# Kernel optimization log

Measured on AMD Instinct MI355X. Metric: run time of the kernel, lower is better.

## Reference

```python
import jax, jax.numpy as jnp
import numpy as np

N_ATOMS, N_EDGES = 8192, 131072
NODE_DIM, HIDDEN_DIM, NUM_BASIS, N_BLOCKS, N_SPECIES = 128, 64, 20, 2, 100
CUTOFF = 5.0


def setup_inputs() -> dict:
    key = jax.random.key(0)
    ks = iter(jax.random.split(key, 40))
    F, H, NB, B, Z = NODE_DIM, HIDDEN_DIM, NUM_BASIS, N_BLOCKS, N_SPECIES

    def w(k, shape, fan_in):
        return jax.random.normal(k, shape, jnp.float32) / np.float32(np.sqrt(fan_in))

    inp = {
        "at_no": jax.random.randint(next(ks), (N_ATOMS,), 1, 86),
        "coord": jax.random.uniform(next(ks), (N_ATOMS, 3), jnp.float32) * 5.0,
        "edge_index": jax.random.randint(next(ks), (2, N_EDGES), 0, N_ATOMS),
        "charge": 0,
        "spin": 0,
        # learned parameters
        "emb": w(next(ks), (Z, F), 1.0),
        "atom_sp": w(next(ks), (Z,), 1.0),
        "msg_w1": w(next(ks), (B, F, F), F), "msg_b1": jnp.zeros((B, F), jnp.float32),
        "msg_w2": w(next(ks), (B, F, 3 * F), F), "msg_b2": jnp.zeros((B, 3 * F), jnp.float32),
        "msg_wr": w(next(ks), (B, NB, 3 * F), NB), "msg_br": jnp.zeros((B, 3 * F), jnp.float32),
        "upd_u": w(next(ks), (B, F, F), F), "upd_v": w(next(ks), (B, F, F), F),
        "upd_w1": w(next(ks), (B, 2 * F, F), 2 * F), "upd_b1": jnp.zeros((B, F), jnp.float32),
        "upd_w2": w(next(ks), (B, F, 3 * F), F), "upd_b2": jnp.zeros((B, 3 * F), jnp.float32),
        "out_w1": w(next(ks), (F, H), F), "out_b1": jnp.zeros((H,), jnp.float32),
        "out_w2": w(next(ks), (H, 1), H), "out_b2": jnp.zeros((1,), jnp.float32),
    }
    return inp


def _painn_energy(coord, at_no, edge_index, emb, atom_sp,
                  msg_w1, msg_b1, msg_w2, msg_b2, msg_wr, msg_br,
                  upd_u, upd_v, upd_w1, upd_b1, upd_w2, upd_b2,
                  out_w1, out_b1, out_w2, out_b2):
    n_atoms = coord.shape[0]
    n_blocks = msg_w1.shape[0]
    nb = msg_wr.shape[1]
    rc = jnp.asarray(CUTOFF, coord.dtype)
    src, dst = edge_index[0], edge_index[1]

    rij = coord[dst] - coord[src]                       # [E,3]
    d = jnp.sqrt(jnp.sum(rij * rij, -1) + 1e-12)        # [E]
    unit = rij / d[:, None]                             # [E,3] (l=1 real sph. harmonics up to const)
    n = jnp.arange(1, nb + 1, dtype=coord.dtype)
    rbf = jnp.sqrt(2.0 / rc) * jnp.sin(n[None, :] * jnp.pi * d[:, None] / rc) / d[:, None]  # Bessel RBF [E,NB]
    fcut = jnp.where(d < rc, 0.5 * (jnp.cos(jnp.pi * d / rc) + 1.0), 0.0)                   # cosine cutoff [E]

    x = emb[at_no]                                      # [N,F]
    v = jnp.zeros((n_atoms, 3, x.shape[1]), x.dtype)    # [N,3,F]

    for b in range(n_blocks):
        # ---- PaiNN message block ----
        phi = jax.nn.silu(x @ msg_w1[b] + msg_b1[b]) @ msg_w2[b] + msg_b2[b]   # [N,3F]
        filt = (rbf @ msg_wr[b] + msg_br[b]) * fcut[:, None]                   # [E,3F]
        m = phi[src] * filt                                                    # [E,3F]
        ds, dv1, dv2 = jnp.split(m, 3, axis=-1)
        dvec = dv1[:, None, :] * v[src] + dv2[:, None, :] * unit[:, :, None]   # [E,3,F]
        x = x + jax.ops.segment_sum(ds, dst, num_segments=n_atoms)
        v = v + jax.ops.segment_sum(dvec, dst, num_segments=n_atoms)
        # ---- PaiNN update block ----
        uv = jnp.einsum('nif,fg->nig', v, upd_u[b])
        vv = jnp.einsum('nif,fg->nig', v, upd_v[b])
        vnorm = jnp.sqrt(jnp.sum(vv * vv, axis=1) + 1e-12)                     # [N,F]
        a = jax.nn.silu(jnp.concatenate([x, vnorm], -1) @ upd_w1[b] + upd_b1[b]) @ upd_w2[b] + upd_b2[b]
        a_vv, a_sv, a_ss = jnp.split(a, 3, axis=-1)
        v = v + a_vv[:, None, :] * uv
        x = x + a_sv * jnp.sum(uv * vv, axis=1) + a_ss

    atom_e = jax.nn.silu(x @ out_w1 + out_b1) @ out_w2 + out_b2                # [N,1]
    return jnp.sum(atom_e) + jnp.sum(atom_sp[at_no])


def reference(at_no, coord, edge_index, charge, spin, emb, atom_sp,
              msg_w1, msg_b1, msg_w2, msg_b2, msg_wr, msg_br,
              upd_u, upd_v, upd_w1, upd_b1, upd_w2, upd_b2,
              out_w1, out_b1, out_w2, out_b2):
    def energy_fn(c):
        return _painn_energy(c, at_no, edge_index, emb, atom_sp,
                             msg_w1, msg_b1, msg_w2, msg_b2, msg_wr, msg_br,
                             upd_u, upd_v, upd_w1, upd_b1, upd_w2, upd_b2,
                             out_w1, out_b1, out_w2, out_b2)
    energy, nuc_grad = jax.value_and_grad(energy_fn)(coord)
    return energy, nuc_grad
```

## Files before the change

### kernel.cpp

```cpp
#include <hip/hip_runtime.h>
#include <math.h>


#define NA 8192
#define NE 131072
#define FD 128
#define FD3 384
#define NBASE 20
#define HD 64
#define RCUT 5.0f
#define PIF 3.14159265358979f

typedef short bf16x8 __attribute__((ext_vector_type(8)));
typedef float f32x4 __attribute__((ext_vector_type(4)));
typedef _Float16 f16x2 __attribute__((ext_vector_type(2)));

static __device__ __forceinline__ float silu_f(float x) {
    return x / (1.f + expf(-x));
}
static __device__ __forceinline__ float dsilu_f(float x) {
    float s = 1.f / (1.f + expf(-x));
    return s * (1.f + x * (1.f - s));
}
static __device__ __forceinline__ short f2bf(float x) {
    union { float f; unsigned int i; } c; c.f = x;
    unsigned int r = c.i + 0x7fffu + ((c.i >> 16) & 1u);
    return (short)(r >> 16);
}
static __device__ __forceinline__ float bf2f(short u) {
    union { unsigned int i; float f; } c; c.i = ((unsigned int)(unsigned short)u) << 16; return c.f;
}
static __device__ __forceinline__ float dot2f(f16x2 a, f16x2 b, float c) {
#if __has_builtin(__builtin_amdgcn_fdot2)
    return __builtin_amdgcn_fdot2(a, b, c, false);
#else
    return c + (float)a.x * (float)b.x + (float)a.y * (float)b.y;
#endif
}
static __device__ __forceinline__ unsigned int packf16(float a, float b) {
    union { _Float16 h[2]; unsigned int u; } c;
    c.h[0] = (_Float16)a; c.h[1] = (_Float16)b;
    return c.u;
}

__global__ __launch_bounds__(256) void mfma_gemm_kernel(
    const float* __restrict__ A, const float* __restrict__ W,
    const float* __restrict__ bias, const float* __restrict__ dsil,
    const float* __restrict__ addbuf, float* __restrict__ C,
    int M, int N, int K, int asilu, int acc, int wtrans)
{
    __shared__ short AsH[128][40];
    __shared__ short AsL[128][40];
    __shared__ short WsH[64][40];
    __shared__ short WsL[64][40];
    int tid = threadIdx.x;
    int row0 = blockIdx.y * 128, col0 = blockIdx.x * 64;
    int wv = tid >> 6, lane = tid & 63;
    int quad = lane >> 4, l16 = lane & 15;

    f32x4 accv[2][4];
    #pragma unroll
    for (int i = 0; i < 2; ++i)
        #pragma unroll
        for (int j = 0; j < 4; ++j) { f32x4 z = {0.f, 0.f, 0.f, 0.f}; accv[i][j] = z; }

    int am = tid >> 1;
    int ak = (tid & 1) * 16;
    const float* abase = A + (size_t)(row0 + am) * K + ak;
    int wn = tid & 63, wk0 = tid >> 6;
    int wk2 = tid & 31, wn2 = tid >> 5;

    for (int k0 = 0; k0 < K; k0 += 32) {
        {
            const float* ap = abase + k0;
            #pragma unroll
            for (int i = 0; i < 4; ++i) {
                float4 v = *(const float4*)(ap + 4 * i);
                if (asilu) {
                    v.x = silu_f(v.x); v.y = silu_f(v.y);
                    v.z = silu_f(v.z); v.w = silu_f(v.w);
                }
                float vv[4] = {v.x, v.y, v.z, v.w};
                #pragma unroll
                for (int q = 0; q < 4; ++q) {
                    short h = f2bf(vv[q]);
                    AsH[am][ak + 4 * i + q] = h;
                    AsL[am][ak + 4 * i + q] = f2bf(vv[q] - bf2f(h));
                }
            }
        }
        if (!wtrans) {
            #pragma unroll
            for (int p = 0; p < 8; ++p) {
                int k = wk0 + p * 4;
                float v = W[(size_t)(k0 + k) * N + col0 + wn];
                short h = f2bf(v);
                WsH[wn][k] = h;
                WsL[wn][k] = f2bf(v - bf2f(h));
            }
        } else {
            #pragma unroll
            for (int p = 0; p < 8; ++p) {
                int n2 = wn2 + p * 8;
                float v = W[(size_t)(col0 + n2) * K + k0 + wk2];
                short h = f2bf(v);
                WsH[n2][wk2] = h;
                WsL[n2][wk2] = f2bf(v - bf2f(h));
            }
        }
        __syncthreads();
        bf16x8 afH[2], afL[2], bfH[4], bfL[4];
        #pragma unroll
        for (int rt = 0; rt < 2; ++rt) {
            afH[rt] = *(const bf16x8*)&AsH[wv * 32 + rt * 16 + l16][quad * 8];
            afL[rt] = *(const bf16x8*)&AsL[wv * 32 + rt * 16 + l16][quad * 8];
        }
        #pragma unroll
        for (int ct = 0; ct < 4; ++ct) {
            bfH[ct] = *(const bf16x8*)&WsH[ct * 16 + l16][quad * 8];
            bfL[ct] = *(const bf16x8*)&WsL[ct * 16 + l16][quad * 8];
        }
        #pragma unroll
        for (int rt = 0; rt < 2; ++rt)
            #pragma unroll
            for (int ct = 0; ct < 4; ++ct) {
                accv[rt][ct] = __builtin_amdgcn_mfma_f32_16x16x32_bf16(
                    afL[rt], bfH[ct], accv[rt][ct], 0, 0, 0);
                accv[rt][ct] = __builtin_amdgcn_mfma_f32_16x16x32_bf16(
                    afH[rt], bfL[ct], accv[rt][ct], 0, 0, 0);
                accv[rt][ct] = __builtin_amdgcn_mfma_f32_16x16x32_bf16(
                    afH[rt], bfH[ct], accv[rt][ct], 0, 0, 0);
            }
        __syncthreads();
    }
    #pragma unroll
    for (int rt = 0; rt < 2; ++rt) {
        #pragma unroll
        for (int ct = 0; ct < 4; ++ct) {
            int colv = col0 + ct * 16 + l16;
            float bv = bias ? bias[colv] : 0.f;
            #pragma unroll
            for (int r = 0; r < 4; ++r) {
                int rowv = row0 + wv * 32 + rt * 16 + quad * 4 + r;
                float v = accv[rt][ct][r] + bv;
                size_t idx = (size_t)rowv * N + colv;
                if (dsil) { float pz = dsil[idx]; float s = 1.f / (1.f + expf(-pz)); v *= s * (1.f + pz * (1.f - s)); }
                if (addbuf) v += addbuf[idx];
                if (acc) C[idx] += v; else C[idx] = v;
            }
        }
    }
}

__global__ void embed_kernel(const int* at_no, const float* emb, float* x) {
    int i = blockIdx.x * blockDim.x + threadIdx.x;
    int n = i >> 7, f = i & 127;
    x[i] = emb[(size_t)at_no[n] * FD + f];
}

__global__ void combo_prep_kernel(const float* u, const float* v, float* UVcomb, float* Tcomb) {
    int i = blockIdx.x * blockDim.x + threadIdx.x;
    {
        int k = i >> 8, j = i & 255;
        UVcomb[i] = (j < 128) ? u[k * 128 + j] : v[k * 128 + (j - 128)];
    }
    {
        int k = i >> 7, j = i & 127;
        Tcomb[i] = (k < 128) ? u[j * 128 + k] : v[j * 128 + (k - 128)];
    }
}

__global__ void wpack_kernel(const float* __restrict__ Wr, unsigned int* __restrict__ out) {
    int i = blockIdx.x * blockDim.x + threadIdx.x;
    if (i >= 3840) return;
    int k2 = i / 384, r = i - k2 * 384;
    out[i] = packf16(Wr[(2 * k2) * FD3 + r], Wr[(2 * k2 + 1) * FD3 + r]);
}

__global__ void geom_fwd_kernel(const float* coord, const int* ei,
    float* d_e, float* unit_e, float* rbf_e, float* drbf_e, float* fcut_e, float* dfc_e,
    unsigned int* rbfh_e, unsigned int* drbfh_e,
    int* cnt_dst, int* cnt_src)
{
    int e = blockIdx.x * blockDim.x + threadIdx.x;
    if (e >= NE) return;
    int s = ei[e], t = ei[NE + e];
    atomicAdd(&cnt_src[s], 1);
    atomicAdd(&cnt_dst[t], 1);
    float rx = coord[t * 3 + 0] - coord[s * 3 + 0];
    float ry = coord[t * 3 + 1] - coord[s * 3 + 1];
    float rz = coord[t * 3 + 2] - coord[s * 3 + 2];
    float r2 = rx * rx + ry * ry + rz * rz;
    float dd = sqrtf(r2 + 1e-12f);
    float inv = 1.f / dd;
    d_e[e] = dd;
    unit_e[e * 3 + 0] = rx * inv; unit_e[e * 3 + 1] = ry * inv; unit_e[e * 3 + 2] = rz * inv;
    const float c0 = 0.6324555320336759f;
    float rb[NBASE], db[NBASE];
    for (int k = 0; k < NBASE; ++k) {
        float nk = (k + 1) * (PIF / RCUT);
        float sn, cs; sincosf(nk * dd, &sn, &cs);
        rb[k] = c0 * sn * inv;
        db[k] = c0 * (nk * cs * inv - sn * inv * inv);
        rbf_e[(size_t)e * NBASE + k] = rb[k];
        drbf_e[(size_t)e * NBASE + k] = db[k];
    }
    #pragma unroll
    for (int k2 = 0; k2 < 10; ++k2) {
        rbfh_e[(size_t)e * 10 + k2] = packf16(rb[2 * k2], rb[2 * k2 + 1]);
        drbfh_e[(size_t)e * 10 + k2] = packf16(db[2 * k2], db[2 * k2 + 1]);
    }
    if (dd < RCUT) {
        float sn, cs; sincosf(PIF * dd / RCUT, &sn, &cs);
        fcut_e[e] = 0.5f * (cs + 1.f);
        dfc_e[e] = -0.5f * (PIF / RCUT) * sn;
    } else { fcut_e[e] = 0.f; dfc_e[e] = 0.f; }
}

__global__ __launch_bounds__(1024) void scan_kernel(
    const int* cnt_dst, const int* cnt_src,
    int* off_dst, int* off_src, int* cur_dst, int* cur_src)
{
    __shared__ int part[1024];
    const int* cnt = (blockIdx.x == 0) ? cnt_dst : cnt_src;
    int* off = (blockIdx.x == 0) ? off_dst : off_src;
    int* cur = (blockIdx.x == 0) ? cur_dst : cur_src;
    int t = threadIdx.x;
    int base = t * 8;
    int loc[8]; int s = 0;
    #pragma unroll
    for (int i = 0; i < 8; ++i) { loc[i] = s; s += cnt[base + i]; }
    part[t] = s;
    __syncthreads();
    for (int d = 1; d < 1024; d <<= 1) {
        int v = part[t];
        int w = (t >= d) ? part[t - d] : 0;
        __syncthreads();
        part[t] = v + w;
        __syncthreads();
    }
    int pre = (t == 0) ? 0 : part[t - 1];
    #pragma unroll
    for (int i = 0; i < 8; ++i) { int o = pre + loc[i]; off[base + i] = o; cur[base + i] = o; }
    if (t == 1023) off[NA] = part[1023];
}

__global__ void scatter_kernel(const int* ei, int* cur_dst, int* cur_src,
                               int* perm_dst, int* perm_src, int* srcp, int* dstp) {
    int e = blockIdx.x * blockDim.x + threadIdx.x;
    if (e >= NE) return;
    int s = ei[e], t = ei[NE + e];
    int pd = atomicAdd(&cur_dst[t], 1); perm_dst[pd] = e; srcp[pd] = s;
    int ps = atomicAdd(&cur_src[s], 1); perm_src[ps] = e; dstp[ps] = t;
}

__global__ __launch_bounds__(256) void msg_fwd_kernel(
    const int* __restrict__ row_off_dst, const int* __restrict__ perm_dst, const int* __restrict__ srcp,
    const unsigned int* __restrict__ rbfh_e, const float* __restrict__ fcut_e, const float* __restrict__ unit_e,
    const float* __restrict__ phi, const unsigned int* __restrict__ Wrp, const float* __restrict__ br,
    const float* __restrict__ x_in, const float* __restrict__ v_in,
    float* __restrict__ x_mid, float* __restrict__ v_mid)
{
    int tid = threadIdx.x;
    int n = blockIdx.x * 2 + (tid >> 7);
    int f = tid & 127;
    f16x2 w0[10], w1[10], w2[10];
    #pragma unroll
    for (int k2 = 0; k2 < 10; ++k2) {
        unsigned int a = Wrp[k2 * 384 + f];
        unsigned int b = Wrp[k2 * 384 + 128 + f];
        unsigned int c = Wrp[k2 * 384 + 256 + f];
        w0[k2] = *(const f16x2*)&a;
        w1[k2] = *(const f16x2*)&b;
        w2[k2] = *(const f16x2*)&c;
    }
    float b0 = br[f], b1 = br[FD + f], b2 = br[2 * FD + f];
    float xa = 0.f, va0 = 0.f, va1 = 0.f, va2 = 0.f;
    int e0 = row_off_dst[n], e1 = row_off_dst[n + 1];
    for (int ii = e0; ii < e1; ++ii) {
        int e = perm_dst[ii];
        int s = srcp[ii];
        float fc = fcut_e[e];
        float raw0 = b0, raw1 = b1, raw2 = b2;
        #pragma unroll
        for (int k2 = 0; k2 < 10; ++k2) {
            unsigned int ra = rbfh_e[(size_t)e * 10 + k2];
            f16x2 r = *(const f16x2*)&ra;
            raw0 = dot2f(r, w0[k2], raw0);
            raw1 = dot2f(r, w1[k2], raw1);
            raw2 = dot2f(r, w2[k2], raw2);
        }
        float f0 = raw0 * fc, f1 = raw1 * fc, f2 = raw2 * fc;
        const float* ph = phi + (size_t)s * FD3;
        float m0 = ph[f] * f0, m1 = ph[FD + f] * f1, m2 = ph[2 * FD + f] * f2;
        xa += m0;
        float u0 = unit_e[e * 3], u1 = unit_e[e * 3 + 1], u2 = unit_e[e * 3 + 2];
        float vs0 = 0.f, vs1 = 0.f, vs2 = 0.f;
        if (v_in) {
            const float* vp = v_in + (size_t)s * 3 * FD;
            vs0 = vp[f]; vs1 = vp[FD + f]; vs2 = vp[2 * FD + f];
        }
        va0 += m1 * vs0 + m2 * u0;
        va1 += m1 * vs1 + m2 * u1;
        va2 += m1 * vs2 + m2 * u2;
    }
    size_t xb = (size_t)n * FD + f;
    x_mid[xb] = x_in[xb] + xa;
    size_t vb = (size_t)n * 3 * FD + f;
    float p0 = 0.f, p1 = 0.f, p2 = 0.f;
    if (v_in) { p0 = v_in[vb]; p1 = v_in[vb + FD]; p2 = v_in[vb + 2 * FD]; }
    v_mid[vb] = p0 + va0; v_mid[vb + FD] = p1 + va1; v_mid[vb + 2 * FD] = p2 + va2;
}

__global__ void vnorm_cat_kernel(const float* xmid, const float* uvvv, float* vnorm, float* cat) {
    int i = blockIdx.x * blockDim.x + threadIdx.x;
    int n = i >> 7, g = i & 127;
    size_t ub = (size_t)n * 3 * 256 + 128 + g;
    float a = uvvv[ub], b = uvvv[ub + 256], c = uvvv[ub + 512];
    float vn = sqrtf(a * a + b * b + c * c + 1e-12f);
    vnorm[i] = vn;
    cat[(size_t)n * 2 * FD + g] = xmid[i];
    cat[(size_t)n * 2 * FD + FD + g] = vn;
}

__global__ void combine_kernel(const float* xmid, const float* vmid,
    const float* uvvv, const float* a_,
    float* x_out, float* v_out )
{
    int i = blockIdx.x * blockDim.x + threadIdx.x;
    int n = i >> 7, g = i & 127;
    size_t vb = (size_t)n * 3 * FD + g;
    size_t ub = (size_t)n * 3 * 256 + g;
    float uv0 = uvvv[ub], uv1 = uvvv[ub + 256], uv2 = uvvv[ub + 512];
    float vv0 = uvvv[ub + 128], vv1 = uvvv[ub + 384], vv2 = uvvv[ub + 640];
    float S = uv0 * vv0 + uv1 * vv1 + uv2 * vv2;
    const float* ar = a_ + (size_t)n * FD3;
    x_out[i] = xmid[i] + ar[FD + g] * S + ar[2 * FD + g];
    if (v_out) {
        float avv = ar[g];
        v_out[vb] = vmid[vb] + avv * uv0;
        v_out[vb + FD] = vmid[vb + FD] + avv * uv1;
        v_out[vb + 2 * FD] = vmid[vb + 2 * FD] + avv * uv2;
    }
}

__global__ __launch_bounds__(256) void energy_kernel(
    const float* tout, const float* ow2, const float* ob2,
    const float* atom_sp, const int* at_no, float* out)
{
    int n = blockIdx.x * 256 + threadIdx.x;
    float e = ob2[0] + atom_sp[at_no[n]];
    for (int h = 0; h < HD; ++h) {
        float t = tout[(size_t)n * HD + h];
        e = fmaf(silu_f(t), ow2[h], e);
    }
    #pragma unroll
    for (int off = 32; off > 0; off >>= 1) e += __shfl_down(e, off);
    __shared__ float s[4];
    int lane = threadIdx.x & 63, wv = threadIdx.x >> 6;
    if (lane == 0) s[wv] = e;
    __syncthreads();
    if (threadIdx.x == 0) atomicAdd(out, s[0] + s[1] + s[2] + s[3]);
}

__global__ __launch_bounds__(128) void head_bwd_kernel(
    const float* tout, const float* ow1, const float* ow2, float* gx)
{
    __shared__ float sh[HD];
    int n = blockIdx.x, f = threadIdx.x;
    if (f < HD) {
        float p = tout[(size_t)n * HD + f];
        sh[f] = dsilu_f(p) * ow2[f];
    }
    __syncthreads();
    float g = 0.f;
    #pragma unroll
    for (int h = 0; h < HD; ++h) g = fmaf(sh[h], ow1[f * HD + h], g);
    gx[(size_t)n * FD + f] = g;
}

__global__ void ubwd1_kernel(const float* gx, const float* gv,
    const float* uvvv, float* g_a)
{
    int i = blockIdx.x * blockDim.x + threadIdx.x;
    int n = i >> 7, g = i & 127;
    size_t vb = (size_t)n * 3 * FD + g;
    size_t ub = (size_t)n * 3 * 256 + g;
    float uv0 = uvvv[ub], uv1 = uvvv[ub + 256], uv2 = uvvv[ub + 512];
    float vv0 = uvvv[ub + 128], vv1 = uvvv[ub + 384], vv2 = uvvv[ub + 640];
    float gv0 = gv[vb], gv1 = gv[vb + FD], gv2 = gv[vb + 2 * FD];
    float gxv = gx[i];
    float S = uv0 * vv0 + uv1 * vv1 + uv2 * vv2;
    size_t ab = (size_t)n * FD3;
    g_a[ab + g]           = gv0 * uv0 + gv1 * uv1 + gv2 * uv2;
    g_a[ab + FD + g]      = gxv * S;
    g_a[ab + 2 * FD + g]  = gxv;
}

__global__ void ubwd2_kernel(const float* gx_in, const float* gv_in,
    const float* a_, const float* vnorm, const float* g_cat,
    float* uvvv, float* gx_mid, float* gv_tmp)
{
    int i = blockIdx.x * blockDim.x + threadIdx.x;
    int n = i >> 7, g = i & 127;
    size_t vb = (size_t)n * 3 * FD + g, ab = (size_t)n * FD3;
    size_t ub = (size_t)n * 3 * 256 + g;
    float gxv = gx_in[i];
    float gS = gxv * a_[ab + FD + g];
    float avv = a_[ab + g];
    float gvn = g_cat[(size_t)n * 2 * FD + FD + g];
    float c = gvn / vnorm[i];
    float uv0 = uvvv[ub], uv1 = uvvv[ub + 256], uv2 = uvvv[ub + 512];
    float vv0 = uvvv[ub + 128], vv1 = uvvv[ub + 384], vv2 = uvvv[ub + 640];
    float gv0 = gv_in[vb], gv1 = gv_in[vb + FD], gv2 = gv_in[vb + 2 * FD];
    uvvv[ub]       = gv0 * avv + gS * vv0;
    uvvv[ub + 256] = gv1 * avv + gS * vv1;
    uvvv[ub + 512] = gv2 * avv + gS * vv2;
    uvvv[ub + 128] = gS * uv0 + c * vv0;
    uvvv[ub + 384] = gS * uv1 + c * vv1;
    uvvv[ub + 640] = gS * uv2 + c * vv2;
    gv_tmp[vb] = gv0; gv_tmp[vb + FD] = gv1; gv_tmp[vb + 2 * FD] = gv2;
    gx_mid[i] = gxv + g_cat[(size_t)n * 2 * FD + g];
}

__global__ __launch_bounds__(256) void msg_bwd_merged_kernel(
    const int* __restrict__ row_off_src, const int* __restrict__ perm_src, const int* __restrict__ dstp,
    const unsigned int* __restrict__ rbfh_e, const unsigned int* __restrict__ drbfh_e,
    const float* __restrict__ fcut_e, const float* __restrict__ dfc_e,
    const float* __restrict__ unit_e,
    const float* phi, const unsigned int* __restrict__ Wrp, const float* __restrict__ br,
    const float* __restrict__ v_in,
    const float* __restrict__ gx_mid, const float* __restrict__ gv_mid,
    float* gphi_out,
    float* __restrict__ gv_out,
    float* __restrict__ gd_e, float* __restrict__ gu_e)
{
    __shared__ float red[12][4][64];
    int tid = threadIdx.x;
    int wv = tid >> 6, lane = tid & 63;
    int n = blockIdx.x;
    f16x2 w[2][3][10];
    float brv[2][3], ph[2][3], vs[2][3];
    #pragma unroll
    for (int h = 0; h < 2; ++h) {
        int f = lane + h * 64;
        #pragma unroll
        for (int s = 0; s < 3; ++s) {
            #pragma unroll
            for (int k2 = 0; k2 < 10; ++k2) {
                unsigned int u = Wrp[k2 * 384 + s * 128 + f];
                w[h][s][k2] = *(const f16x2*)&u;
            }
            brv[h][s] = br[s * FD + f];
            ph[h][s] = phi[(size_t)n * FD3 + s * FD + f];
            vs[h][s] = v_in ? v_in[(size_t)n * 3 * FD + s * FD + f] : 0.f;
        }
    }
    float gp[2][3] = {{0.f, 0.f, 0.f}, {0.f, 0.f, 0.f}};
    float ga[2][3] = {{0.f, 0.f, 0.f}, {0.f, 0.f, 0.f}};
    int e0 = row_off_src[n], e1 = row_off_src[n + 1];
    for (int ii = e0 + wv; ii < e1; ii += 4) {
        int e = perm_src[ii], dd = dstp[ii];
        float fc = fcut_e[e], dfc = dfc_e[e];
        float u0 = unit_e[e * 3], u1 = unit_e[e * 3 + 1], u2 = unit_e[e * 3 + 2];
        f16x2 rb2[10], db2[10];
        #pragma unroll
        for (int k2 = 0; k2 < 10; ++k2) {
            unsigned int ra = rbfh_e[(size_t)e * 10 + k2];
            unsigned int db = drbfh_e[(size_t)e * 10 + k2];
            rb2[k2] = *(const f16x2*)&ra;
            db2[k2] = *(const f16x2*)&db;
        }
        float r0 = 0.f, r1 = 0.f, r2 = 0.f, r3 = 0.f;
        #pragma unroll
        for (int h = 0; h < 2; ++h) {
            int f = lane + h * 64;
            float raw0 = brv[h][0], raw1 = brv[h][1], raw2 = brv[h][2];
            float A0 = 0.f, A1 = 0.f, A2 = 0.f;
            #pragma unroll
            for (int k2 = 0; k2 < 10; ++k2) {
                raw0 = dot2f(rb2[k2], w[h][0][k2], raw0);
                raw1 = dot2f(rb2[k2], w[h][1][k2], raw1);
                raw2 = dot2f(rb2[k2], w[h][2][k2], raw2);
                A0 = dot2f(db2[k2], w[h][0][k2], A0);
                A1 = dot2f(db2[k2], w[h][1][k2], A1);
                A2 = dot2f(db2[k2], w[h][2][k2], A2);
            }
            float f0 = raw0 * fc, f1 = raw1 * fc, f2 = raw2 * fc;
            float gds = gx_mid[(size_t)dd * FD + f];
            const float* gvp = gv_mid + (size_t)dd * 3 * FD;
            float gd0 = gvp[f], gd1 = gvp[FD + f], gd2 = gvp[2 * FD + f];
            float gdv1 = gd0 * vs[h][0] + gd1 * vs[h][1] + gd2 * vs[h][2];
            float gdv2 = gd0 * u0 + gd1 * u1 + gd2 * u2;
            float dv1 = ph[h][1] * f1;
            ga[h][0] += gd0 * dv1; ga[h][1] += gd1 * dv1; ga[h][2] += gd2 * dv1;
            gp[h][0] += gds * f0; gp[h][1] += gdv1 * f1; gp[h][2] += gdv2 * f2;
            float dv2 = ph[h][2] * f2;
            r1 += gd0 * dv2; r2 += gd1 * dv2; r3 += gd2 * dv2;
            float gf0 = gds * ph[h][0], gf1 = gdv1 * ph[h][1], gf2 = gdv2 * ph[h][2];
            r0 += fc * (gf0 * A0 + gf1 * A1 + gf2 * A2)
                + dfc * (gf0 * raw0 + gf1 * raw1 + gf2 * raw2);
        }
        #pragma unroll
        for (int off = 32; off > 0; off >>= 1) {
            r0 += __shfl_down(r0, off);
            r1 += __shfl_down(r1, off);
            r2 += __shfl_down(r2, off);
            r3 += __shfl_down(r3, off);
        }
        if (lane == 0) {
            gd_e[e] += r0;
            gu_e[e * 3]     += r1;
            gu_e[e * 3 + 1] += r2;
            gu_e[e * 3 + 2] += r3;
        }
    }
    #pragma unroll
    for (int h = 0; h < 2; ++h)
        #pragma unroll
        for (int s = 0; s < 3; ++s) {
            red[h * 3 + s][wv][lane] = gp[h][s];
            red[6 + h * 3 + s][wv][lane] = ga[h][s];
        }
    __syncthreads();
    int j0 = tid >> 6;
    #pragma unroll
    for (int rep = 0; rep < 3; ++rep) {
        int j = j0 + rep * 4;
        float v = red[j][0][lane] + red[j][1][lane] + red[j][2][lane] + red[j][3][lane];
        int jj = (j < 6) ? j : j - 6;
        int h = jj / 3, s = jj - 3 * h;
        int f = h * 64 + lane;
        if (j < 6) {
            gphi_out[(size_t)n * FD3 + s * FD + f] = v;
        } else {
            size_t vb = (size_t)n * 3 * FD + s * FD + f;
            gv_out[vb] = gv_mid[vb] + v;
        }
    }
}

__global__ void edge_vec_kernel(const float* coord, const int* ei,
    const float* d_e, const float* gd_e, const float* gu_e, float* gvec)
{
    int e = blockIdx.x * blockDim.x + threadIdx.x;
    if (e >= NE) return;
    int s = ei[e], t = ei[NE + e];
    float rx = coord[t * 3 + 0] - coord[s * 3 + 0];
    float ry = coord[t * 3 + 1] - coord[s * 3 + 1];
    float rz = coord[t * 3 + 2] - coord[s * 3 + 2];
    float dd = d_e[e];
    float inv = 1.f / dd;
    float gu0 = gu_e[e * 3], gu1 = gu_e[e * 3 + 1], gu2 = gu_e[e * 3 + 2];
    float gd = gd_e[e];
    float dot = gu0 * rx + gu1 * ry + gu2 * rz;
    float coef = gd * inv - dot * inv * inv * inv;
    gvec[e * 3 + 0] = gu0 * inv + coef * rx;
    gvec[e * 3 + 1] = gu1 * inv + coef * ry;
    gvec[e * 3 + 2] = gu2 * inv + coef * rz;
}

__global__ __launch_bounds__(256) void coord_gather_kernel(
    const int* __restrict__ off_dst, const int* __restrict__ perm_dst,
    const int* __restrict__ off_src, const int* __restrict__ perm_src,
    const float* __restrict__ gvec, float* __restrict__ gcoord)
{
    int n = blockIdx.x * 4 + (threadIdx.x >> 6);
    int lane = threadIdx.x & 63;
    float a0 = 0.f, a1 = 0.f, a2 = 0.f;
    int d0 = off_dst[n], d1 = off_dst[n + 1];
    for (int ii = d0 + lane; ii < d1; ii += 64) {
        int e = perm_dst[ii];
        a0 += gvec[e * 3]; a1 += gvec[e * 3 + 1]; a2 += gvec[e * 3 + 2];
    }
    int s0 = off_src[n], s1 = off_src[n + 1];
    for (int ii = s0 + lane; ii < s1; ii += 64) {
        int e = perm_src[ii];
        a0 -= gvec[e * 3]; a1 -= gvec[e * 3 + 1]; a2 -= gvec[e * 3 + 2];
    }
    #pragma unroll
    for (int off = 32; off > 0; off >>= 1) {
        a0 += __shfl_down(a0, off);
        a1 += __shfl_down(a1, off);
        a2 += __shfl_down(a2, off);
    }
    if (lane == 0) {
        gcoord[n * 3 + 0] = a0; gcoord[n * 3 + 1] = a1; gcoord[n * 3 + 2] = a2;
    }
}

extern "C" void kernel_launch(void* const* d_in, const int* in_sizes, int n_in,
                              void* d_out, int out_size, void* d_ws, size_t ws_size,
                              hipStream_t stream)
{
    (void)in_sizes; (void)n_in; (void)out_size; (void)ws_size;
    const int*   at_no   = (const int*)  d_in[0];
    const float* coord   = (const float*)d_in[1];
    const int*   eidx    = (const int*)  d_in[2];
    const float* emb     = (const float*)d_in[5];
    const float* atom_sp = (const float*)d_in[6];
    const float* msg_w1  = (const float*)d_in[7];
    const float* msg_b1  = (const float*)d_in[8];
    const float* msg_w2  = (const float*)d_in[9];
    const float* msg_b2  = (const float*)d_in[10];
    const float* msg_wr  = (const float*)d_in[11];
    const float* msg_br  = (const float*)d_in[12];
    const float* upd_u   = (const float*)d_in[13];
    const float* upd_v   = (const float*)d_in[14];
    const float* upd_w1  = (const float*)d_in[15];
    const float* upd_b1  = (const float*)d_in[16];
    const float* upd_w2  = (const float*)d_in[17];
    const float* upd_b2  = (const float*)d_in[18];
    const float* out_w1  = (const float*)d_in[19];
    const float* out_b1  = (const float*)d_in[20];
    const float* out_w2  = (const float*)d_in[21];
    const float* out_b2  = (const float*)d_in[22];
    float* out = (float*)d_out;
    float* gcoord = out + 1;

    char* wp = (char*)d_ws;
    auto alloc = [&](size_t nelem) -> float* {
        float* r = (float*)wp; wp += ((nelem * 4 + 255) & ~(size_t)255); return r;
    };
    auto alloci = [&](size_t nelem) -> int* {
        int* r = (int*)wp; wp += ((nelem * 4 + 255) & ~(size_t)255); return r;
    };
    auto allocu = [&](size_t nelem) -> unsigned int* {
        unsigned int* r = (unsigned int*)wp; wp += ((nelem * 4 + 255) & ~(size_t)255); return r;
    };
    const size_t NF = (size_t)NA * FD;

    float* d_e    = alloc(NE);
    float* unit_e = alloc(3 * (size_t)NE);
    float* rbf_e  = alloc((size_t)NBASE * NE);
    float* drbf_e = alloc((size_t)NBASE * NE);
    float* fcut_e = alloc(NE);
    float* dfc_e  = alloc(NE);
    float* gd_e   = alloc(NE);
    float* gu_e   = alloc(3 * (size_t)NE);
    unsigned int* rbfh_e  = allocu((size_t)10 * NE);
    unsigned int* drbfh_e = allocu((size_t)10 * NE);
    int* cnt_dst = alloci(NA); int* cnt_src = alloci(NA);
    int* off_dst = alloci(NA + 1); int* off_src = alloci(NA + 1);
    int* cur_dst = alloci(NA); int* cur_src = alloci(NA);
    int* perm_dst = alloci(NE); int* perm_src = alloci(NE);
    int* srcp = alloci(NE); int* dstp = alloci(NE);
    float* xin_all = alloc(3 * NF);
    float* xin0 = xin_all; float* xin1 = xin_all + NF; float* xfin = xin_all + 2 * NF;
    float* vout0 = alloc(3 * NF);
    float* xmid = alloc(NF);
    float* vmid = alloc(3 * NF);
    float* catb = alloc(2 * NF);
    float* toutb = alloc((size_t)NA * HD);
    float *s1b[2], *phib[2], *uvvv[2], *vnb[2], *t1b[2], *ab[2];
    for (int b = 0; b < 2; ++b) {
        s1b[b] = alloc(NF); phib[b] = alloc(3 * NF); uvvv[b] = alloc(6 * NF);
        vnb[b] = alloc(NF); t1b[b] = alloc(NF); ab[b] = alloc(3 * NF);
    }
    float* gxA = alloc(NF); float* gxB = alloc(NF);
    float* gvA = alloc(3 * NF);
    float* g_a   = xin_all;
    float* g_cat = catb;
    float* g_t1  = xmid;
    float* g_s1  = s1b[0];
    float* gvec_e = gu_e;
    float *UVcomb[2], *Tcomb[2];
    for (int b = 0; b < 2; ++b) { UVcomb[b] = alloc(FD * 256); Tcomb[b] = alloc(256 * FD); }
    unsigned int* Wrp[2];
    for (int b = 0; b < 2; ++b) Wrp[b] = allocu(3840);

    hipMemsetAsync(d_out, 0, (size_t)(1 + NA * 3) * 4, stream);
    hipMemsetAsync(cnt_dst, 0, (size_t)NA * 4, stream);
    hipMemsetAsync(cnt_src, 0, (size_t)NA * 4, stream);
    hipMemsetAsync(gd_e, 0, (size_t)NE * 4, stream);
    hipMemsetAsync(gu_e, 0, 3ull * NE * 4, stream);
    hipMemsetAsync(gvA, 0, 3 * NF * 4, stream);

    geom_fwd_kernel<<<NE / 256, 256, 0, stream>>>(coord, eidx, d_e, unit_e, rbf_e, drbf_e,
                                                  fcut_e, dfc_e, rbfh_e, drbfh_e, cnt_dst, cnt_src);
    scan_kernel<<<2, 1024, 0, stream>>>(cnt_dst, cnt_src, off_dst, off_src, cur_dst, cur_src);
    scatter_kernel<<<NE / 256, 256, 0, stream>>>(eidx, cur_dst, cur_src, perm_dst, perm_src, srcp, dstp);
    embed_kernel<<<NF / 256, 256, 0, stream>>>(at_no, emb, xin0);
    for (int b = 0; b < 2; ++b) {
        combo_prep_kernel<<<128, 256, 0, stream>>>(upd_u + (size_t)b * FD * FD,
                                                   upd_v + (size_t)b * FD * FD, UVcomb[b], Tcomb[b]);
        wpack_kernel<<<15, 256, 0, stream>>>(msg_wr + (size_t)b * NBASE * FD3, Wrp[b]);
    }

    auto gemm = [&](const float* A, const float* W, const float* bias, const float* dsil,
                    const float* addb, float* C, int M, int Nn, int K, int asilu, int acc, int wtrans) {
        dim3 g(Nn / 64, M / 128);
        mfma_gemm_kernel<<<g, 256, 0, stream>>>(A, W, bias, dsil, addb, C, M, Nn, K, asilu, acc, wtrans);
    };

    for (int b = 0; b < 2; ++b) {
        const float* xinb = b ? xin1 : xin0;
        const float* vin  = b ? vout0 : nullptr;
        gemm(xinb, msg_w1 + (size_t)b * FD * FD, msg_b1 + b * FD, nullptr, nullptr, s1b[b], NA, FD, FD, 0, 0, 0);
        gemm(s1b[b], msg_w2 + (size_t)b * FD * FD3, msg_b2 + b * FD3, nullptr, nullptr, phib[b], NA, FD3, FD, 1, 0, 0);
        msg_fwd_kernel<<<NA / 2, 256, 0, stream>>>(off_dst, perm_dst, srcp, rbfh_e, fcut_e, unit_e,
                                              phib[b], Wrp[b], msg_br + (size_t)b * FD3,
                                              xinb, vin, xmid, vmid);
        gemm(vmid, UVcomb[b], nullptr, nullptr, nullptr, uvvv[b], 3 * NA, 256, FD, 0, 0, 0);
        vnorm_cat_kernel<<<NF / 256, 256, 0, stream>>>(xmid, uvvv[b], vnb[b], catb);
        gemm(catb, upd_w1 + (size_t)b * 2 * FD * FD, upd_b1 + b * FD, nullptr, nullptr, t1b[b], NA, FD, 2 * FD, 0, 0, 0);
        gemm(t1b[b], upd_w2 + (size_t)b * FD * FD3, upd_b2 + b * FD3, nullptr, nullptr, ab[b], NA, FD3, FD, 1, 0, 0);
        combine_kernel<<<NF / 256, 256, 0, stream>>>(xmid, vmid, uvvv[b], ab[b],
                                                     b ? xfin : xin1, b ? nullptr : vout0);
    }
    gemm(xfin, out_w1, out_b1, nullptr, nullptr, toutb, NA, HD, FD, 0, 0, 0);
    energy_kernel<<<NA / 256, 256, 0, stream>>>(toutb, out_w2, out_b2, atom_sp, at_no, out);

    head_bwd_kernel<<<NA, FD, 0, stream>>>(toutb, out_w1, out_w2, gxA);
    for (int b = 1; b >= 0; --b) {
        ubwd1_kernel<<<NF / 256, 256, 0, stream>>>(gxA, gvA, uvvv[b], g_a);
        gemm(g_a, upd_w2 + (size_t)b * FD * FD3, nullptr, t1b[b], nullptr, g_t1, NA, FD, FD3, 0, 0, 1);
        gemm(g_t1, upd_w1 + (size_t)b * 2 * FD * FD, nullptr, nullptr, nullptr, g_cat, NA, 2 * FD, FD, 0, 0, 1);
        ubwd2_kernel<<<NF / 256, 256, 0, stream>>>(gxA, gvA, ab[b], vnb[b], g_cat,
                                                   uvvv[b], gxB, vmid);
        gemm(uvvv[b], Tcomb[b], nullptr, nullptr, nullptr, vmid, 3 * NA, FD, 256, 0, 1, 0);
        msg_bwd_merged_kernel<<<NA, 256, 0, stream>>>(off_src, perm_src, dstp,
                                              rbfh_e, drbfh_e, fcut_e, dfc_e, unit_e,
                                              phib[b], Wrp[b], msg_br + (size_t)b * FD3,
                                              b ? vout0 : nullptr, gxB, vmid,
                                              phib[b], gvA, gd_e, gu_e);
        if (b == 1) {
            gemm(phib[b], msg_w2 + (size_t)b * FD * FD3, nullptr, s1b[b], nullptr, g_s1, NA, FD, FD3, 0, 0, 1);
            gemm(g_s1, msg_w1 + (size_t)b * FD * FD, nullptr, nullptr, gxB, gxA, NA, FD, FD, 0, 0, 1);
        }
    }
    edge_vec_kernel<<<NE / 256, 256, 0, stream>>>(coord, eidx, d_e, gd_e, gu_e, gvec_e);
    coord_gather_kernel<<<NA / 4, 256, 0, stream>>>(off_dst, perm_dst, off_src, perm_src, gvec_e, gcoord);
}
```

Baseline: 1.165 ms.

## Add 64-row GEMM tile for small-N GEMMs and pack edge geometry into float4

Adds a 64x64-tile split-bf16 MFMA GEMM, used for the M=8192, N<=128 GEMMs, so these small GEMMs launch more blocks and fill more of the GPU's compute units. Packs each edge's unit vector and cutoff into one float4, so the message kernels fetch them with a single vector load instead of four scattered loads. Stops writing the fp32 rbf/drbf arrays, which no kernel reads, cutting geometry-kernel store traffic. The smaller tile reuses each loaded weight tile across fewer rows.

```diff
diff --git a/kernel.cpp b/kernel.cpp
--- a/kernel.cpp
+++ b/kernel.cpp
@@ -152,6 +152,103 @@
     }
 }
 
+__global__ __launch_bounds__(256) void mfma_gemm64_kernel(
+    const float* __restrict__ A, const float* __restrict__ W,
+    const float* __restrict__ bias, const float* __restrict__ dsil,
+    const float* __restrict__ addbuf, float* __restrict__ C,
+    int M, int N, int K, int asilu, int acc, int wtrans)
+{
+    __shared__ short AsH[64][40];
+    __shared__ short AsL[64][40];
+    __shared__ short WsH[64][40];
+    __shared__ short WsL[64][40];
+    int tid = threadIdx.x;
+    int row0 = blockIdx.y * 64, col0 = blockIdx.x * 64;
+    int wv = tid >> 6, lane = tid & 63;
+    int quad = lane >> 4, l16 = lane & 15;
+
+    f32x4 accv[4];
+    #pragma unroll
+    for (int j = 0; j < 4; ++j) { f32x4 z = {0.f, 0.f, 0.f, 0.f}; accv[j] = z; }
+
+    int am = tid >> 2;
+    int ak = (tid & 3) * 8;
+    const float* abase = A + (size_t)(row0 + am) * K + ak;
+    int wn = tid & 63, wk0 = tid >> 6;
+    int wk2 = tid & 31, wn2 = tid >> 5;
+
+    for (int k0 = 0; k0 < K; k0 += 32) {
+        {
+            const float* ap = abase + k0;
+            #pragma unroll
+            for (int i = 0; i < 2; ++i) {
+                float4 v = *(const float4*)(ap + 4 * i);
+                if (asilu) {
+                    v.x = silu_f(v.x); v.y = silu_f(v.y);
+                    v.z = silu_f(v.z); v.w = silu_f(v.w);
+                }
+                float vv[4] = {v.x, v.y, v.z, v.w};
+                #pragma unroll
+                for (int q = 0; q < 4; ++q) {
+                    short h = f2bf(vv[q]);
+                    AsH[am][ak + 4 * i + q] = h;
+                    AsL[am][ak + 4 * i + q] = f2bf(vv[q] - bf2f(h));
+                }
+            }
+        }
+        if (!wtrans) {
+            #pragma unroll
+            for (int p = 0; p < 8; ++p) {
+                int k = wk0 + p * 4;
+                float v = W[(size_t)(k0 + k) * N + col0 + wn];
+                short h = f2bf(v);
+                WsH[wn][k] = h;
+                WsL[wn][k] = f2bf(v - bf2f(h));
+            }
+        } else {
+            #pragma unroll
+            for (int p = 0; p < 8; ++p) {
+                int n2 = wn2 + p * 8;
+                float v = W[(size_t)(col0 + n2) * K + k0 + wk2];
+                short h = f2bf(v);
+                WsH[n2][wk2] = h;
+                WsL[n2][wk2] = f2bf(v - bf2f(h));
+            }
+        }
+        __syncthreads();
+        bf16x8 afH, afL, bfH[4], bfL[4];
+        afH = *(const bf16x8*)&AsH[wv * 16 + l16][quad * 8];
+        afL = *(const bf16x8*)&AsL[wv * 16 + l16][quad * 8];
+        #pragma unroll
+        for (int ct = 0; ct < 4; ++ct) {
+            bfH[ct] = *(const bf16x8*)&WsH[ct * 16 + l16][quad * 8];
+            bfL[ct] = *(const bf16x8*)&WsL[ct * 16 + l16][quad * 8];
+        }
+        #pragma unroll
+        for (int ct = 0; ct < 4; ++ct) {
+            accv[ct] = __builtin_amdgcn_mfma_f32_16x16x32_bf16(afL, bfH[ct], accv[ct], 0, 0, 0);
+            accv[ct] = __builtin_amdgcn_mfma_f32_16x16x32_bf16(afH, bfL[ct], accv[ct], 0, 0, 0);
+            accv[ct] = __builtin_amdgcn_mfma_f32_16x16x32_bf16(afH, bfH[ct], accv[ct], 0, 0, 0);
+        }
+        __syncthreads();
+    }
+    #pragma unroll
+    for (int ct = 0; ct < 4; ++ct) {
+        int colv = col0 + ct * 16 + l16;
+        if (colv >= N) continue;
+        float bv = bias ? bias[colv] : 0.f;
+        #pragma unroll
+        for (int r = 0; r < 4; ++r) {
+            int rowv = row0 + wv * 16 + quad * 4 + r;
+            float v = accv[ct][r] + bv;
+            size_t idx = (size_t)rowv * N + colv;
+            if (dsil) { float pz = dsil[idx]; float s = 1.f / (1.f + expf(-pz)); v *= s * (1.f + pz * (1.f - s)); }
+            if (addbuf) v += addbuf[idx];
+            if (acc) C[idx] += v; else C[idx] = v;
+        }
+    }
+}
+
 __global__ void embed_kernel(const int* at_no, const float* emb, float* x) {
     int i = blockIdx.x * blockDim.x + threadIdx.x;
     int n = i >> 7, f = i & 127;
@@ -178,7 +275,7 @@
 }
 
 __global__ void geom_fwd_kernel(const float* coord, const int* ei,
-    float* d_e, float* unit_e, float* rbf_e, float* drbf_e, float* fcut_e, float* dfc_e,
+    float* d_e, float4* geo4, float* dfc_e,
     unsigned int* rbfh_e, unsigned int* drbfh_e,
     int* cnt_dst, int* cnt_src)
 {
@@ -194,7 +291,6 @@
     float dd = sqrtf(r2 + 1e-12f);
     float inv = 1.f / dd;
     d_e[e] = dd;
-    unit_e[e * 3 + 0] = rx * inv; unit_e[e * 3 + 1] = ry * inv; unit_e[e * 3 + 2] = rz * inv;
     const float c0 = 0.6324555320336759f;
     float rb[NBASE], db[NBASE];
     for (int k = 0; k < NBASE; ++k) {
@@ -202,19 +298,21 @@
         float sn, cs; sincosf(nk * dd, &sn, &cs);
         rb[k] = c0 * sn * inv;
         db[k] = c0 * (nk * cs * inv - sn * inv * inv);
-        rbf_e[(size_t)e * NBASE + k] = rb[k];
-        drbf_e[(size_t)e * NBASE + k] = db[k];
     }
     #pragma unroll
     for (int k2 = 0; k2 < 10; ++k2) {
         rbfh_e[(size_t)e * 10 + k2] = packf16(rb[2 * k2], rb[2 * k2 + 1]);
         drbfh_e[(size_t)e * 10 + k2] = packf16(db[2 * k2], db[2 * k2 + 1]);
     }
+    float fc = 0.f, dfc = 0.f;
     if (dd < RCUT) {
         float sn, cs; sincosf(PIF * dd / RCUT, &sn, &cs);
-        fcut_e[e] = 0.5f * (cs + 1.f);
-        dfc_e[e] = -0.5f * (PIF / RCUT) * sn;
-    } else { fcut_e[e] = 0.f; dfc_e[e] = 0.f; }
+        fc = 0.5f * (cs + 1.f);
+        dfc = -0.5f * (PIF / RCUT) * sn;
+    }
+    float4 g; g.x = rx * inv; g.y = ry * inv; g.z = rz * inv; g.w = fc;
+    geo4[e] = g;
+    dfc_e[e] = dfc;
 }
 
 __global__ __launch_bounds__(1024) void scan_kernel(
@@ -256,7 +354,7 @@
 
 __global__ __launch_bounds__(256) void msg_fwd_kernel(
     const int* __restrict__ row_off_dst, const int* __restrict__ perm_dst, const int* __restrict__ srcp,
-    const unsigned int* __restrict__ rbfh_e, const float* __restrict__ fcut_e, const float* __restrict__ unit_e,
+    const unsigned int* __restrict__ rbfh_e, const float4* __restrict__ geo4,
     const float* __restrict__ phi, const unsigned int* __restrict__ Wrp, const float* __restrict__ br,
     const float* __restrict__ x_in, const float* __restrict__ v_in,
     float* __restrict__ x_mid, float* __restrict__ v_mid)
@@ -280,7 +378,8 @@
     for (int ii = e0; ii < e1; ++ii) {
         int e = perm_dst[ii];
         int s = srcp[ii];
-        float fc = fcut_e[e];
+        float4 g = geo4[e];
+        float fc = g.w;
         float raw0 = b0, raw1 = b1, raw2 = b2;
         #pragma unroll
         for (int k2 = 0; k2 < 10; ++k2) {
@@ -294,15 +393,14 @@
         const float* ph = phi + (size_t)s * FD3;
         float m0 = ph[f] * f0, m1 = ph[FD + f] * f1, m2 = ph[2 * FD + f] * f2;
         xa += m0;
-        float u0 = unit_e[e * 3], u1 = unit_e[e * 3 + 1], u2 = unit_e[e * 3 + 2];
         float vs0 = 0.f, vs1 = 0.f, vs2 = 0.f;
         if (v_in) {
             const float* vp = v_in + (size_t)s * 3 * FD;
             vs0 = vp[f]; vs1 = vp[FD + f]; vs2 = vp[2 * FD + f];
         }
-        va0 += m1 * vs0 + m2 * u0;
-        va1 += m1 * vs1 + m2 * u1;
-        va2 += m1 * vs2 + m2 * u2;
+        va0 += m1 * vs0 + m2 * g.x;
+        va1 += m1 * vs1 + m2 * g.y;
+        va2 += m1 * vs2 + m2 * g.z;
     }
     size_t xb = (size_t)n * FD + f;
     x_mid[xb] = x_in[xb] + xa;
@@ -426,8 +524,7 @@
 __global__ __launch_bounds__(256) void msg_bwd_merged_kernel(
     const int* __restrict__ row_off_src, const int* __restrict__ perm_src, const int* __restrict__ dstp,
     const unsigned int* __restrict__ rbfh_e, const unsigned int* __restrict__ drbfh_e,
-    const float* __restrict__ fcut_e, const float* __restrict__ dfc_e,
-    const float* __restrict__ unit_e,
+    const float4* __restrict__ geo4, const float* __restrict__ dfc_e,
     const float* phi, const unsigned int* __restrict__ Wrp, const float* __restrict__ br,
     const float* __restrict__ v_in,
     const float* __restrict__ gx_mid, const float* __restrict__ gv_mid,
@@ -461,8 +558,8 @@
     int e0 = row_off_src[n], e1 = row_off_src[n + 1];
     for (int ii = e0 + wv; ii < e1; ii += 4) {
         int e = perm_src[ii], dd = dstp[ii];
-        float fc = fcut_e[e], dfc = dfc_e[e];
-        float u0 = unit_e[e * 3], u1 = unit_e[e * 3 + 1], u2 = unit_e[e * 3 + 2];
+        float4 g = geo4[e];
+        float fc = g.w, dfc = dfc_e[e];
         f16x2 rb2[10], db2[10];
         #pragma unroll
         for (int k2 = 0; k2 < 10; ++k2) {
@@ -491,7 +588,7 @@
             const float* gvp = gv_mid + (size_t)dd * 3 * FD;
             float gd0 = gvp[f], gd1 = gvp[FD + f], gd2 = gvp[2 * FD + f];
             float gdv1 = gd0 * vs[h][0] + gd1 * vs[h][1] + gd2 * vs[h][2];
-            float gdv2 = gd0 * u0 + gd1 * u1 + gd2 * u2;
+            float gdv2 = gd0 * g.x + gd1 * g.y + gd2 * g.z;
             float dv1 = ph[h][1] * f1;
             ga[h][0] += gd0 * dv1; ga[h][1] += gd1 * dv1; ga[h][2] += gd2 * dv1;
             gp[h][0] += gds * f0; gp[h][1] += gdv1 * f1; gp[h][2] += gdv2 * f2;
@@ -631,10 +728,7 @@
     const size_t NF = (size_t)NA * FD;
 
     float* d_e    = alloc(NE);
-    float* unit_e = alloc(3 * (size_t)NE);
-    float* rbf_e  = alloc((size_t)NBASE * NE);
-    float* drbf_e = alloc((size_t)NBASE * NE);
-    float* fcut_e = alloc(NE);
+    float4* geo4  = (float4*)alloc(4 * (size_t)NE);
     float* dfc_e  = alloc(NE);
     float* gd_e   = alloc(NE);
     float* gu_e   = alloc(3 * (size_t)NE);
@@ -676,8 +770,8 @@
     hipMemsetAsync(gu_e, 0, 3ull * NE * 4, stream);
     hipMemsetAsync(gvA, 0, 3 * NF * 4, stream);
 
-    geom_fwd_kernel<<<NE / 256, 256, 0, stream>>>(coord, eidx, d_e, unit_e, rbf_e, drbf_e,
-                                                  fcut_e, dfc_e, rbfh_e, drbfh_e, cnt_dst, cnt_src);
+    geom_fwd_kernel<<<NE / 256, 256, 0, stream>>>(coord, eidx, d_e, geo4, dfc_e,
+                                                  rbfh_e, drbfh_e, cnt_dst, cnt_src);
     scan_kernel<<<2, 1024, 0, stream>>>(cnt_dst, cnt_src, off_dst, off_src, cur_dst, cur_src);
     scatter_kernel<<<NE / 256, 256, 0, stream>>>(eidx, cur_dst, cur_src, perm_dst, perm_src, srcp, dstp);
     embed_kernel<<<NF / 256, 256, 0, stream>>>(at_no, emb, xin0);
@@ -689,8 +783,13 @@
 
     auto gemm = [&](const float* A, const float* W, const float* bias, const float* dsil,
                     const float* addb, float* C, int M, int Nn, int K, int asilu, int acc, int wtrans) {
-        dim3 g(Nn / 64, M / 128);
-        mfma_gemm_kernel<<<g, 256, 0, stream>>>(A, W, bias, dsil, addb, C, M, Nn, K, asilu, acc, wtrans);
+        if (M == NA && Nn <= 128) {
+            dim3 g((Nn + 63) / 64, M / 64);
+            mfma_gemm64_kernel<<<g, 256, 0, stream>>>(A, W, bias, dsil, addb, C, M, Nn, K, asilu, acc, wtrans);
+        } else {
+            dim3 g(Nn / 64, M / 128);
+            mfma_gemm_kernel<<<g, 256, 0, stream>>>(A, W, bias, dsil, addb, C, M, Nn, K, asilu, acc, wtrans);
+        }
     };
 
     for (int b = 0; b < 2; ++b) {
@@ -698,7 +797,7 @@
         const float* vin  = b ? vout0 : nullptr;
         gemm(xinb, msg_w1 + (size_t)b * FD * FD, msg_b1 + b * FD, nullptr, nullptr, s1b[b], NA, FD, FD, 0, 0, 0);
         gemm(s1b[b], msg_w2 + (size_t)b * FD * FD3, msg_b2 + b * FD3, nullptr, nullptr, phib[b], NA, FD3, FD, 1, 0, 0);
-        msg_fwd_kernel<<<NA / 2, 256, 0, stream>>>(off_dst, perm_dst, srcp, rbfh_e, fcut_e, unit_e,
+        msg_fwd_kernel<<<NA / 2, 256, 0, stream>>>(off_dst, perm_dst, srcp, rbfh_e, geo4,
                                               phib[b], Wrp[b], msg_br + (size_t)b * FD3,
                                               xinb, vin, xmid, vmid);
         gemm(vmid, UVcomb[b], nullptr, nullptr, nullptr, uvvv[b], 3 * NA, 256, FD, 0, 0, 0);
@@ -720,7 +819,7 @@
                                                    uvvv[b], gxB, vmid);
         gemm(uvvv[b], Tcomb[b], nullptr, nullptr, nullptr, vmid, 3 * NA, FD, 256, 0, 1, 0);
         msg_bwd_merged_kernel<<<NA, 256, 0, stream>>>(off_src, perm_src, dstp,
-                                              rbfh_e, drbfh_e, fcut_e, dfc_e, unit_e,
+                                              rbfh_e, drbfh_e, geo4, dfc_e,
                                               phib[b], Wrp[b], msg_br + (size_t)b * FD3,
                                               b ? vout0 : nullptr, gxB, vmid,
                                               phib[b], gvA, gd_e, gu_e);
```

Result: faster. 1.011 ms (median of 2 runs) (-13.2%).
